# Optimization experiments

Measured on AMD Instinct MI355X. Metric: run time of the kernel, lower is better.

## Reference

```python
import jax, jax.numpy as jnp
import numpy as np

B, S, D, H = 4, 2048, 512, 8
HD = D // H
POOL_HEADS = 8


def setup_inputs() -> dict:
    key = jax.random.key(0)
    ks = iter(jax.random.split(key, 32))
    p = {}
    p['x'] = jax.random.normal(next(ks), (B, S, D), dtype=jnp.float32)
    p['mask'] = jnp.zeros((B, S), dtype=jnp.float32)  # key_padding_mask (1.0 = padded)
    s = 1.0 / np.sqrt(D)
    for layer in ('1', '2'):
        for name in ('q', 'k', 'v', 'o'):
            p[f'{name}{layer}_w'] = jax.random.normal(next(ks), (D, D), dtype=jnp.float32) * s
            p[f'{name}{layer}_b'] = jnp.zeros((D,), dtype=jnp.float32)
    p['ln1_g'] = jnp.ones((D,), jnp.float32); p['ln1_b'] = jnp.zeros((D,), jnp.float32)
    p['ffn_w1'] = jax.random.normal(next(ks), (D, D), dtype=jnp.float32) * s
    p['ffn_b1'] = jnp.zeros((D,), jnp.float32)
    p['ffn_w2'] = jax.random.normal(next(ks), (D, D), dtype=jnp.float32) * s
    p['ffn_b2'] = jnp.zeros((D,), jnp.float32)
    p['ln2_g'] = jnp.ones((D,), jnp.float32); p['ln2_b'] = jnp.zeros((D,), jnp.float32)
    p['pool_w'] = jax.random.normal(next(ks), (D, POOL_HEADS), dtype=jnp.float32) * s
    p['pool_b'] = jnp.zeros((POOL_HEADS,), jnp.float32)
    return p


def _layernorm(x, g, b, eps=1e-5):
    mu = jnp.mean(x, axis=-1, keepdims=True)
    var = jnp.var(x, axis=-1, keepdims=True)
    return (x - mu) * jax.lax.rsqrt(var + eps) * g + b


def _mha(x, mask, qw, qb, kw, kb, vw, vb, ow, ob):
    b, s, d = x.shape
    q = (x @ qw + qb).reshape(b, s, H, HD)
    k = (x @ kw + kb).reshape(b, s, H, HD)
    v = (x @ vw + vb).reshape(b, s, H, HD)
    scores = jnp.einsum('bihd,bjhd->bhij', q, k) / jnp.sqrt(jnp.float32(HD))
    scores = scores - mask[:, None, None, :] * 1e30  # key_padding_mask
    w = jax.nn.softmax(scores, axis=-1)  # dropout is identity at eval
    out = jnp.einsum('bhij,bjhd->bihd', w, v).reshape(b, s, d)
    return out @ ow + ob


def _pool(x, mask, pw, pb):
    alpha = jax.nn.leaky_relu(x @ pw + pb)            # [B,S,POOL_HEADS]
    alpha = alpha + mask[:, :, None] * -1e16
    alpha = jax.nn.softmax(alpha, axis=1)             # softmax over sequence
    # sum over heads of alpha_h * x, then sum over sequence
    return jnp.einsum('bs,bsd->bd', alpha.sum(axis=-1), x)


def reference(x, mask,
              q1_w, q1_b, k1_w, k1_b, v1_w, v1_b, o1_w, o1_b,
              q2_w, q2_b, k2_w, k2_b, v2_w, v2_b, o2_w, o2_b,
              ln1_g, ln1_b, ffn_w1, ffn_b1, ffn_w2, ffn_b2,
              ln2_g, ln2_b, pool_w, pool_b):
    # F.normalize(x, p=2, dim=-1)
    x = x / jnp.maximum(jnp.linalg.norm(x, axis=-1, keepdims=True), 1e-12)
    h = _mha(x, mask, q1_w, q1_b, k1_w, k1_b, v1_w, v1_b, o1_w, o1_b)
    h = _layernorm(h, ln1_g, ln1_b)
    h = jax.nn.relu(h @ ffn_w1 + ffn_b1) @ ffn_w2 + ffn_b2
    h = _mha(h, mask, q2_w, q2_b, k2_w, k2_b, v2_w, v2_b, o2_w, o2_b)
    h = _layernorm(h, ln2_g, ln2_b)
    return _pool(h, mask, pool_w, pool_b)  # [B, D] patch_feature (cls=False -> logit is None)
```

## Files before the change

kernel.cpp:

```cpp
#include <hip/hip_runtime.h>
#include <hip/hip_bf16.h>
#include <stdint.h>

#define DEVI __device__ __forceinline__

typedef float f32x4 __attribute__((ext_vector_type(4)));
typedef short bf16x8 __attribute__((ext_vector_type(8)));

typedef __attribute__((address_space(3))) unsigned int as3_u32;
typedef __attribute__((address_space(1))) unsigned int as1_u32;

DEVI void gload16(const void* g, void* l) {
  __builtin_amdgcn_global_load_lds((const as1_u32*)g, (as3_u32*)l, 16, 0, 0);
}

DEVI unsigned short bf16r(float f) {
  union { float f; unsigned int u; } v; v.f = f;
  unsigned int u = v.u;
  return (unsigned short)((u + 0x7FFFu + ((u >> 16) & 1u)) >> 16);
}

struct PrepArgs {
  const float* w[10];
  const float* b1[3];
  const float* b2[3];
};

__global__ __launch_bounds__(256) void prep_kernel(PrepArgs pa, unsigned short* wt,
                                                   float* qb1, float* qb2) {
  __shared__ float lt[64][65];
  const int slot = blockIdx.z;
  const int n0 = blockIdx.x * 64, k0 = blockIdx.y * 64;
  const float* W = pa.w[slot];
  for (int it = 0; it < 16; it++) {
    int idx = it * 256 + threadIdx.x;
    int kr = idx >> 6, nc = idx & 63;
    lt[kr][nc] = W[(long)(k0 + kr) * 512 + n0 + nc];
  }
  __syncthreads();
  unsigned short* dst = wt + (long)slot * 512 * 512;
  for (int it = 0; it < 16; it++) {
    int idx = it * 256 + threadIdx.x;
    int nr = idx >> 6, kc = idx & 63;
    dst[(long)(n0 + nr) * 512 + k0 + kc] = bf16r(lt[kc][nr]);
  }
  if (blockIdx.x == 0 && blockIdx.y == 0) {
    if (slot < 3) {
      for (int i = threadIdx.x; i < 512; i += 256) qb1[slot * 512 + i] = pa.b1[slot][i];
    } else if (slot >= 6 && slot < 9) {
      for (int i = threadIdx.x; i < 512; i += 256) qb2[(slot - 6) * 512 + i] = pa.b2[slot - 6][i];
    }
  }
}

__global__ __launch_bounds__(256) void l2norm_kernel(const float* __restrict__ x,
                                                     unsigned short* __restrict__ xn) {
  const long row = blockIdx.x;
  const float* xr = x + row * 512;
  float v0 = xr[threadIdx.x], v1 = xr[threadIdx.x + 256];
  float ss = v0 * v0 + v1 * v1;
  #pragma unroll
  for (int off = 32; off > 0; off >>= 1) ss += __shfl_down(ss, off, 64);
  __shared__ float red[4];
  __shared__ float sc[1];
  int w = threadIdx.x >> 6, ln = threadIdx.x & 63;
  if (ln == 0) red[w] = ss;
  __syncthreads();
  if (threadIdx.x == 0) {
    float S = red[0] + red[1] + red[2] + red[3];
    sc[0] = 1.0f / fmaxf(sqrtf(S), 1e-12f);
  }
  __syncthreads();
  float s = sc[0];
  xn[row * 512 + threadIdx.x] = bf16r(v0 * s);
  xn[row * 512 + threadIdx.x + 256] = bf16r(v1 * s);
}

template <int EPI>
__global__ __launch_bounds__(256) void gemm_bt(const unsigned short* __restrict__ A,
                                               const unsigned short* __restrict__ Bt,
                                               const float* __restrict__ bias,
                                               void* __restrict__ Cv, int K, int N) {
  __shared__ unsigned short ldsA[128 * 64];
  __shared__ unsigned short ldsB[128 * 64];
  const int tid = threadIdx.x, w = tid >> 6, ln = tid & 63;
  const int bm = blockIdx.x, bn = blockIdx.y;
  const int wm = (w >> 1) * 64, wn = (w & 1) * 64;
  const f32x4 zf = {0.f, 0.f, 0.f, 0.f};
  f32x4 acc[4][4];
  #pragma unroll
  for (int i = 0; i < 4; i++)
    #pragma unroll
    for (int j = 0; j < 4; j++) acc[i][j] = zf;
  const int r8 = ln >> 3, s8 = ln & 7;
  for (int kt = 0; kt < K; kt += 64) {
    #pragma unroll
    for (int i = 0; i < 4; i++) {
      int row = w * 32 + i * 8 + r8;
      gload16(A + (long)(bm * 128 + row) * K + kt + s8 * 8, &ldsA[(w * 32 + i * 8) * 64]);
      gload16(Bt + (long)(bn * 128 + row) * K + kt + s8 * 8, &ldsB[(w * 32 + i * 8) * 64]);
    }
    __syncthreads();
    #pragma unroll
    for (int kk = 0; kk < 2; kk++) {
      bf16x8 af[4], bfr[4];
      #pragma unroll
      for (int mf = 0; mf < 4; mf++) {
        int row = wm + mf * 16 + (ln & 15);
        af[mf] = *(const bf16x8*)&ldsA[row * 64 + kk * 32 + (ln >> 4) * 8];
      }
      #pragma unroll
      for (int nf = 0; nf < 4; nf++) {
        int row = wn + nf * 16 + (ln & 15);
        bfr[nf] = *(const bf16x8*)&ldsB[row * 64 + kk * 32 + (ln >> 4) * 8];
      }
      #pragma unroll
      for (int mf = 0; mf < 4; mf++)
        #pragma unroll
        for (int nf = 0; nf < 4; nf++)
          acc[mf][nf] = __builtin_amdgcn_mfma_f32_16x16x32_bf16(af[mf], bfr[nf], acc[mf][nf], 0, 0, 0);
    }
    __syncthreads();
  }
  const int g = ln >> 4, c = ln & 15;
  #pragma unroll
  for (int mf = 0; mf < 4; mf++) {
    #pragma unroll
    for (int nf = 0; nf < 4; nf++) {
      int col = bn * 128 + wn + nf * 16 + c;
      float bv = bias[col];
      #pragma unroll
      for (int j = 0; j < 4; j++) {
        long row = bm * 128 + wm + mf * 16 + g * 4 + j;
        float v = acc[mf][nf][j] + bv;
        if (EPI == 2) v = v > 0.f ? v : 0.f;
        if (EPI == 0)
          ((float*)Cv)[row * N + col] = v;
        else
          ((unsigned short*)Cv)[row * N + col] = bf16r(v);
      }
    }
  }
}

__global__ __launch_bounds__(256) void vtrans_kernel(const unsigned short* __restrict__ v,
                                                     unsigned short* __restrict__ vt) {
  __shared__ unsigned short lt[64][72];
  const int bh = blockIdx.x;
  const int st = blockIdx.y * 64;
  const unsigned short* src = v + (long)((bh >> 3) * 2048 + st) * 1536 + (bh & 7) * 64;
  for (int it = 0; it < 16; it++) {
    int idx = it * 256 + threadIdx.x;
    int r = idx >> 6, cc = idx & 63;
    lt[r][cc] = src[(long)r * 1536 + cc];
  }
  __syncthreads();
  unsigned short* dst = vt + (long)bh * 64 * 2048 + st;
  for (int it = 0; it < 16; it++) {
    int idx = it * 256 + threadIdx.x;
    int dr = idx >> 6, sc = idx & 63;
    dst[(long)dr * 2048 + sc] = lt[sc][dr];
  }
}

__global__ __launch_bounds__(256, 4) void attn_split_kernel(
    const unsigned short* __restrict__ qkv,
    const unsigned short* __restrict__ vt,
    const float* __restrict__ mask,
    float* __restrict__ opart,
    float* __restrict__ lpart) {
  const int tid = threadIdx.x, w = tid >> 6, ln = tid & 63;
  const int g = ln >> 4, c = ln & 15;
  const int bh = blockIdx.y, b = bh >> 3, h = bh & 7;
  const int sp = blockIdx.z;
  const int q0 = blockIdx.x * 128 + w * 32;
  const unsigned short* qp = qkv + (long)(b * 2048) * 1536 + h * 64;
  const unsigned short* kp = qp + 512;
  const unsigned short* vtp = vt + (long)bh * 64 * 2048;
  const float* mp = mask + b * 2048;

  __shared__ unsigned short kbuf[2][32 * 64];
  __shared__ unsigned short vbuf[2][64 * 32];
  __shared__ unsigned short pbuf[4 * 16 * 64];
  unsigned short* pb = &pbuf[w * 1024];

  const int jj0 = w * 2;
  auto stage = [&](int buf, int kt) {
    #pragma unroll
    for (int u = 0; u < 2; u++) {
      int jj = jj0 + u;
      if (jj < 4) {
        int r = jj * 8 + (ln >> 3);
        int s = ln & 7;
        gload16(kp + (long)(kt + r) * 1536 + ((s ^ (r & 7)) * 8),
                &kbuf[buf][jj * 512]);
      } else {
        int j = jj - 4;
        int r = j * 16 + (ln >> 2);
        int s = ln & 3;
        gload16(vtp + (long)r * 2048 + kt + ((s ^ ((r >> 1) & 3)) * 8),
                &vbuf[buf][j * 512]);
      }
    }
  };

  const f32x4 zf = {0.f, 0.f, 0.f, 0.f};
  bf16x8 qf[2][2];
  #pragma unroll
  for (int qi = 0; qi < 2; qi++)
    #pragma unroll
    for (int kk = 0; kk < 2; kk++)
      qf[qi][kk] = *(const bf16x8*)(qp + (long)(q0 + qi * 16 + c) * 1536 + kk * 32 + g * 8);

  f32x4 of[4][2];
  #pragma unroll
  for (int i = 0; i < 4; i++)
    #pragma unroll
    for (int j = 0; j < 2; j++) of[i][j] = zf;
  float lsum[2] = {0.f, 0.f};

  const int kt0 = sp * 1024;
  stage(0, kt0);
  __syncthreads();

  for (int it = 0; it < 32; it++) {
    const int kt = kt0 + it * 32;
    const int cur = it & 1;
    if (it + 1 < 32) stage(cur ^ 1, kt + 32);
    float mval = mp[kt + (ln & 31)];
    bf16x8 kf[2][2];
    #pragma unroll
    for (int ki = 0; ki < 2; ki++)
      #pragma unroll
      for (int kk = 0; kk < 2; kk++)
        kf[ki][kk] = *(const bf16x8*)&kbuf[cur][(ki * 16 + c) * 64 + (((kk * 4 + g) ^ (c & 7)) * 8)];
    bf16x8 vf[4];
    #pragma unroll
    for (int hf = 0; hf < 4; hf++)
      vf[hf] = *(const bf16x8*)&vbuf[cur][(hf * 16 + c) * 32 + ((g ^ ((c >> 1) & 3)) * 8)];
    f32x4 st[2][2];
    #pragma unroll
    for (int ki = 0; ki < 2; ki++)
      #pragma unroll
      for (int qi = 0; qi < 2; qi++) {
        f32x4 t0 = __builtin_amdgcn_mfma_f32_16x16x32_bf16(kf[ki][0], qf[qi][0], zf, 0, 0, 0);
        st[ki][qi] = __builtin_amdgcn_mfma_f32_16x16x32_bf16(kf[ki][1], qf[qi][1], t0, 0, 0, 0);
      }
    float madj[2][4];
    #pragma unroll
    for (int ki = 0; ki < 2; ki++)
      #pragma unroll
      for (int j = 0; j < 4; j++) madj[ki][j] = 0.f;
    if (__any(mval != 0.f)) {
      #pragma unroll
      for (int ki = 0; ki < 2; ki++)
        #pragma unroll
        for (int j = 0; j < 4; j++)
          madj[ki][j] = -1.4426950408889634e30f * __shfl(mval, ki * 16 + g * 4 + j, 64);
    }
    const float SC = 0.18033688011112042f;
    #pragma unroll
    for (int qi = 0; qi < 2; qi++) {
      #pragma unroll
      for (int ki = 0; ki < 2; ki++) {
        float e0 = __builtin_amdgcn_exp2f(st[ki][qi][0] * SC + madj[ki][0]);
        float e1 = __builtin_amdgcn_exp2f(st[ki][qi][1] * SC + madj[ki][1]);
        float e2 = __builtin_amdgcn_exp2f(st[ki][qi][2] * SC + madj[ki][2]);
        float e3 = __builtin_amdgcn_exp2f(st[ki][qi][3] * SC + madj[ki][3]);
        lsum[qi] += (e0 + e1) + (e2 + e3);
        __hip_bfloat162 h01 = __float22bfloat162_rn(make_float2(e0, e1));
        __hip_bfloat162 h23 = __float22bfloat162_rn(make_float2(e2, e3));
        uint2 pk;
        pk.x = *(unsigned int*)&h01;
        pk.y = *(unsigned int*)&h23;
        int slot = (qi * 4 + ki * 2 + (g >> 1)) ^ (c & 7);
        *(uint2*)&pb[c * 64 + slot * 8 + (g & 1) * 4] = pk;
      }
    }
    bf16x8 pfr[2];
    #pragma unroll
    for (int qi = 0; qi < 2; qi++) {
      int slot = (qi * 4 + g) ^ (c & 7);
      pfr[qi] = *(const bf16x8*)&pb[c * 64 + slot * 8];
    }
    #pragma unroll
    for (int hf = 0; hf < 4; hf++)
      #pragma unroll
      for (int qi = 0; qi < 2; qi++)
        of[hf][qi] = __builtin_amdgcn_mfma_f32_16x16x32_bf16(vf[hf], pfr[qi], of[hf][qi], 0, 0, 0);
    __syncthreads();
  }
  #pragma unroll
  for (int qi = 0; qi < 2; qi++) {
    lsum[qi] += __shfl_xor(lsum[qi], 16, 64);
    lsum[qi] += __shfl_xor(lsum[qi], 32, 64);
  }
  float* ob = opart + (long)(sp * 32 + bh) * 2048 * 64;
  #pragma unroll
  for (int qi = 0; qi < 2; qi++) {
    long row = q0 + qi * 16 + c;
    #pragma unroll
    for (int hf = 0; hf < 4; hf++)
      *(f32x4*)(ob + row * 64 + hf * 16 + g * 4) = of[hf][qi];
  }
  if (g == 0) {
    #pragma unroll
    for (int qi = 0; qi < 2; qi++)
      lpart[(long)(sp * 32 + bh) * 2048 + q0 + qi * 16 + c] = lsum[qi];
  }
}

__global__ __launch_bounds__(256) void attn_combine(const float* __restrict__ opart,
                                                    const float* __restrict__ lpart,
                                                    unsigned short* __restrict__ ao) {
  const long row = blockIdx.x;
  const int b = (int)(row >> 11), q = (int)(row & 2047);
  #pragma unroll
  for (int half = 0; half < 2; half++) {
    int col = threadIdx.x + half * 256;
    int h = col >> 6, hd = col & 63;
    int bh = b * 8 + h;
    float l = lpart[(long)bh * 2048 + q] + lpart[(long)(32 + bh) * 2048 + q];
    long i0 = ((long)bh * 2048 + q) * 64 + hd;
    long i1 = ((long)(32 + bh) * 2048 + q) * 64 + hd;
    float v = (opart[i0] + opart[i1]) / l;
    ao[row * 512 + col] = bf16r(v);
  }
}

template <int OUTF>
__global__ __launch_bounds__(256) void ln_kernel(const float* __restrict__ in,
                                                 const float* __restrict__ gam,
                                                 const float* __restrict__ bet,
                                                 void* __restrict__ out) {
  const long row = blockIdx.x;
  const float* x = in + row * 512;
  float v0 = x[threadIdx.x], v1 = x[threadIdx.x + 256];
  float s = v0 + v1, ss = v0 * v0 + v1 * v1;
  #pragma unroll
  for (int off = 32; off > 0; off >>= 1) {
    s += __shfl_down(s, off, 64);
    ss += __shfl_down(ss, off, 64);
  }
  __shared__ float red[8];
  __shared__ float mv[2];
  int w = threadIdx.x >> 6, ln = threadIdx.x & 63;
  if (ln == 0) { red[w] = s; red[w + 4] = ss; }
  __syncthreads();
  if (threadIdx.x == 0) {
    float S = red[0] + red[1] + red[2] + red[3];
    float SS = red[4] + red[5] + red[6] + red[7];
    float mu = S * (1.f / 512.f);
    float var = SS * (1.f / 512.f) - mu * mu;
    mv[0] = mu;
    mv[1] = rsqrtf(var + 1e-5f);
  }
  __syncthreads();
  float mu = mv[0], rs = mv[1];
  float o0 = (v0 - mu) * rs * gam[threadIdx.x] + bet[threadIdx.x];
  float o1 = (v1 - mu) * rs * gam[threadIdx.x + 256] + bet[threadIdx.x + 256];
  if (OUTF == 0) {
    ((unsigned short*)out)[row * 512 + threadIdx.x] = bf16r(o0);
    ((unsigned short*)out)[row * 512 + threadIdx.x + 256] = bf16r(o1);
  } else {
    ((float*)out)[row * 512 + threadIdx.x] = o0;
    ((float*)out)[row * 512 + threadIdx.x + 256] = o1;
  }
}

__global__ __launch_bounds__(256) void alpha_kernel(const float* __restrict__ h,
                                                    const float* __restrict__ pw,
                                                    const float* __restrict__ pbias,
                                                    const float* __restrict__ mask,
                                                    float* __restrict__ alpha) {
  int w = threadIdx.x >> 6, ln = threadIdx.x & 63;
  long row = (long)blockIdx.x * 4 + w;
  float p[8];
  #pragma unroll
  for (int k = 0; k < 8; k++) p[k] = 0.f;
  #pragma unroll
  for (int it = 0; it < 8; it++) {
    int d = it * 64 + ln;
    float xv = h[row * 512 + d];
    const float* wr = pw + d * 8;
    #pragma unroll
    for (int k = 0; k < 8; k++) p[k] += xv * wr[k];
  }
  #pragma unroll
  for (int off = 32; off > 0; off >>= 1)
    #pragma unroll
    for (int k = 0; k < 8; k++) p[k] += __shfl_down(p[k], off, 64);
  if (ln == 0) {
    float mterm = mask[row] * (-1e16f);
    #pragma unroll
    for (int k = 0; k < 8; k++) {
      float a = p[k] + pbias[k];
      a = a < 0.f ? 0.01f * a : a;
      alpha[row * 8 + k] = a + mterm;
    }
  }
}

__global__ __launch_bounds__(256) void stats_kernel(const float* __restrict__ alpha,
                                                    float* __restrict__ stats) {
  int b = blockIdx.x >> 3, ph = blockIdx.x & 7;
  const float* a = alpha + (long)b * 2048 * 8 + ph;
  __shared__ float rr[4];
  __shared__ float mm[1];
  int w = threadIdx.x >> 6, ln = threadIdx.x & 63;
  float m = -1e38f;
  for (int s = threadIdx.x; s < 2048; s += 256) m = fmaxf(m, a[(long)s * 8]);
  #pragma unroll
  for (int off = 32; off > 0; off >>= 1) m = fmaxf(m, __shfl_down(m, off, 64));
  if (ln == 0) rr[w] = m;
  __syncthreads();
  if (threadIdx.x == 0) mm[0] = fmaxf(fmaxf(rr[0], rr[1]), fmaxf(rr[2], rr[3]));
  __syncthreads();
  float M = mm[0];
  float sum = 0.f;
  for (int s = threadIdx.x; s < 2048; s += 256) sum += __expf(a[(long)s * 8] - M);
  #pragma unroll
  for (int off = 32; off > 0; off >>= 1) sum += __shfl_down(sum, off, 64);
  __syncthreads();
  if (ln == 0) rr[w] = sum;
  __syncthreads();
  if (threadIdx.x == 0) {
    stats[blockIdx.x * 2] = M;
    stats[blockIdx.x * 2 + 1] = rr[0] + rr[1] + rr[2] + rr[3];
  }
}

__global__ __launch_bounds__(256) void pool_kernel(const float* __restrict__ h,
                                                   const float* __restrict__ alpha,
                                                   const float* __restrict__ stats,
                                                   float* __restrict__ partial) {
  int b = blockIdx.x >> 3, sc = blockIdx.x & 7;
  int s0 = sc * 256;
  __shared__ float wb[256];
  {
    long s = s0 + threadIdx.x;
    const float* a = alpha + ((long)b * 2048 + s) * 8;
    float wsum = 0.f;
    #pragma unroll
    for (int ph = 0; ph < 8; ph++) {
      float M = stats[(b * 8 + ph) * 2], Sm = stats[(b * 8 + ph) * 2 + 1];
      wsum += __expf(a[ph] - M) / Sm;
    }
    wb[threadIdx.x] = wsum;
  }
  __syncthreads();
  float a0 = 0.f, a1 = 0.f;
  const float* hb = h + ((long)b * 2048 + s0) * 512;
  for (int i = 0; i < 256; i++) {
    float wv = wb[i];
    a0 += wv * hb[(long)i * 512 + threadIdx.x];
    a1 += wv * hb[(long)i * 512 + threadIdx.x + 256];
  }
  partial[(long)blockIdx.x * 512 + threadIdx.x] = a0;
  partial[(long)blockIdx.x * 512 + threadIdx.x + 256] = a1;
}

__global__ __launch_bounds__(256) void pool_final(const float* __restrict__ partial,
                                                  float* __restrict__ out) {
  int b = blockIdx.x;
  float a0 = 0.f, a1 = 0.f;
  #pragma unroll
  for (int sc = 0; sc < 8; sc++) {
    a0 += partial[(long)(b * 8 + sc) * 512 + threadIdx.x];
    a1 += partial[(long)(b * 8 + sc) * 512 + threadIdx.x + 256];
  }
  out[b * 512 + threadIdx.x] = a0;
  out[b * 512 + threadIdx.x + 256] = a1;
}

extern "C" void kernel_launch(void* const* d_in, const int* in_sizes, int n_in,
                              void* d_out, int out_size, void* d_ws, size_t ws_size,
                              hipStream_t stream) {
  (void)in_sizes; (void)n_in; (void)out_size;
  if (ws_size < 92274688UL) return;

  const float* x    = (const float*)d_in[0];
  const float* mask = (const float*)d_in[1];
  const float* q1w = (const float*)d_in[2];  const float* q1b = (const float*)d_in[3];
  const float* k1w = (const float*)d_in[4];  const float* k1b = (const float*)d_in[5];
  const float* v1w = (const float*)d_in[6];  const float* v1b = (const float*)d_in[7];
  const float* o1w = (const float*)d_in[8];  const float* o1b = (const float*)d_in[9];
  const float* q2w = (const float*)d_in[10]; const float* q2b = (const float*)d_in[11];
  const float* k2w = (const float*)d_in[12]; const float* k2b = (const float*)d_in[13];
  const float* v2w = (const float*)d_in[14]; const float* v2b = (const float*)d_in[15];
  const float* o2w = (const float*)d_in[16]; const float* o2b = (const float*)d_in[17];
  const float* ln1g = (const float*)d_in[18]; const float* ln1b = (const float*)d_in[19];
  const float* fw1 = (const float*)d_in[20]; const float* fb1 = (const float*)d_in[21];
  const float* fw2 = (const float*)d_in[22]; const float* fb2 = (const float*)d_in[23];
  const float* ln2g = (const float*)d_in[24]; const float* ln2b = (const float*)d_in[25];
  const float* poolw = (const float*)d_in[26]; const float* poolb = (const float*)d_in[27];

  char* ws = (char*)d_ws;
  unsigned short* Wt  = (unsigned short*)(ws + 0);
  float* qb1          = (float*)(ws + 5242880);
  float* qb2          = (float*)(ws + 5249024);
  float* stats        = (float*)(ws + 5255168);
  float* alpha        = (float*)(ws + 5255424);
  float* partial      = (float*)(ws + 5517568);
  unsigned short* qkv = (unsigned short*)(ws + 8388608);
  unsigned short* vt  = (unsigned short*)(ws + 33554432);
  unsigned short* ao  = (unsigned short*)(ws + 41943040);
  float* t            = (float*)(ws + 50331648);
  unsigned short* xn  = (unsigned short*)(ws + 67108864);
  unsigned short* h1  = (unsigned short*)(ws + 75497472);
  unsigned short* f   = (unsigned short*)(ws + 83886080);
  unsigned short* h2  = xn;
  float* opart        = (float*)(ws + 50331648);
  float* lpart        = (float*)(ws + 83886080);

  PrepArgs pa;
  pa.w[0] = q1w; pa.w[1] = k1w; pa.w[2] = v1w; pa.w[3] = o1w; pa.w[4] = fw1;
  pa.w[5] = fw2; pa.w[6] = q2w; pa.w[7] = k2w; pa.w[8] = v2w; pa.w[9] = o2w;
  pa.b1[0] = q1b; pa.b1[1] = k1b; pa.b1[2] = v1b;
  pa.b2[0] = q2b; pa.b2[1] = k2b; pa.b2[2] = v2b;

  prep_kernel<<<dim3(8, 8, 10), 256, 0, stream>>>(pa, Wt, qb1, qb2);
  l2norm_kernel<<<8192, 256, 0, stream>>>(x, xn);

  gemm_bt<1><<<dim3(64, 12), 256, 0, stream>>>(xn, Wt, qb1, qkv, 512, 1536);
  vtrans_kernel<<<dim3(32, 32), 256, 0, stream>>>(qkv + 1024, vt);
  attn_split_kernel<<<dim3(16, 32, 2), 256, 0, stream>>>(qkv, vt, mask, opart, lpart);
  attn_combine<<<8192, 256, 0, stream>>>(opart, lpart, ao);
  gemm_bt<0><<<dim3(64, 4), 256, 0, stream>>>(ao, Wt + 3L * 512 * 512, o1b, t, 512, 512);
  ln_kernel<0><<<8192, 256, 0, stream>>>(t, ln1g, ln1b, h1);
  gemm_bt<2><<<dim3(64, 4), 256, 0, stream>>>(h1, Wt + 4L * 512 * 512, fb1, f, 512, 512);
  gemm_bt<1><<<dim3(64, 4), 256, 0, stream>>>(f, Wt + 5L * 512 * 512, fb2, h2, 512, 512);

  gemm_bt<1><<<dim3(64, 12), 256, 0, stream>>>(h2, Wt + 6L * 512 * 512, qb2, qkv, 512, 1536);
  vtrans_kernel<<<dim3(32, 32), 256, 0, stream>>>(qkv + 1024, vt);
  attn_split_kernel<<<dim3(16, 32, 2), 256, 0, stream>>>(qkv, vt, mask, opart, lpart);
  attn_combine<<<8192, 256, 0, stream>>>(opart, lpart, ao);
  gemm_bt<0><<<dim3(64, 4), 256, 0, stream>>>(ao, Wt + 9L * 512 * 512, o2b, t, 512, 512);
  ln_kernel<1><<<8192, 256, 0, stream>>>(t, ln2g, ln2b, t);

  alpha_kernel<<<2048, 256, 0, stream>>>(t, poolw, poolb, mask, alpha);
  stats_kernel<<<32, 256, 0, stream>>>(alpha, stats);
  pool_kernel<<<32, 256, 0, stream>>>(t, alpha, stats, partial);
  pool_final<<<4, 256, 0, stream>>>(partial, (float*)d_out);
}
```

Measured before the change: 309.6 us.

## Fuse V transpose into QKV GEMM, widen attention K tile, add 64-wide GEMM

The QKV GEMM now writes V columns directly in transposed [b,h,hd,s] layout through a new epilogue mode, which removes the separate vtrans kernel and its extra read and write of V. The attention kernel stages 64 keys per buffer instead of 32. That halves the number of barriers and stage calls, but doubles the LDS used for K and V. The 512-wide GEMMs switch to a 128x64 tile variant, which doubles the grid from 256 to 512 blocks for better CU occupancy at the cost of less data reuse per block.

```diff
diff --git a/kernel.cpp b/kernel.cpp
--- a/kernel.cpp
+++ b/kernel.cpp
@@ -80,7 +80,8 @@
 __global__ __launch_bounds__(256) void gemm_bt(const unsigned short* __restrict__ A,
                                                const unsigned short* __restrict__ Bt,
                                                const float* __restrict__ bias,
-                                               void* __restrict__ Cv, int K, int N) {
+                                               void* __restrict__ Cv, int K, int N,
+                                               unsigned short* __restrict__ vtout) {
   __shared__ unsigned short ldsA[128 * 64];
   __shared__ unsigned short ldsB[128 * 64];
   const int tid = threadIdx.x, w = tid >> 6, ln = tid & 63;
@@ -128,6 +129,85 @@
     #pragma unroll
     for (int nf = 0; nf < 4; nf++) {
       int col = bn * 128 + wn + nf * 16 + c;
+      float bv = bias[col];
+      if (EPI == 3 && col >= 1024) {
+        long row0 = bm * 128 + wm + mf * 16 + g * 4;
+        int b = (int)(row0 >> 11), s = (int)(row0 & 2047);
+        int vc = col - 1024, h = vc >> 6, hd = vc & 63;
+        ushort4 o;
+        o.x = bf16r(acc[mf][nf][0] + bv);
+        o.y = bf16r(acc[mf][nf][1] + bv);
+        o.z = bf16r(acc[mf][nf][2] + bv);
+        o.w = bf16r(acc[mf][nf][3] + bv);
+        *(ushort4*)(vtout + ((long)((b * 8 + h) * 64 + hd)) * 2048 + s) = o;
+      } else {
+        #pragma unroll
+        for (int j = 0; j < 4; j++) {
+          long row = bm * 128 + wm + mf * 16 + g * 4 + j;
+          float v = acc[mf][nf][j] + bv;
+          if (EPI == 2) v = v > 0.f ? v : 0.f;
+          if (EPI == 0)
+            ((float*)Cv)[row * N + col] = v;
+          else
+            ((unsigned short*)Cv)[row * N + col] = bf16r(v);
+        }
+      }
+    }
+  }
+}
+
+template <int EPI>
+__global__ __launch_bounds__(256) void gemm_bt64(const unsigned short* __restrict__ A,
+                                                 const unsigned short* __restrict__ Bt,
+                                                 const float* __restrict__ bias,
+                                                 void* __restrict__ Cv, int K, int N) {
+  __shared__ unsigned short ldsA[128 * 64];
+  __shared__ unsigned short ldsB[64 * 64];
+  const int tid = threadIdx.x, w = tid >> 6, ln = tid & 63;
+  const int bm = blockIdx.x, bn = blockIdx.y;
+  const int wm = (w >> 1) * 64, wn = (w & 1) * 32;
+  const f32x4 zf = {0.f, 0.f, 0.f, 0.f};
+  f32x4 acc[4][2];
+  #pragma unroll
+  for (int i = 0; i < 4; i++)
+    #pragma unroll
+    for (int j = 0; j < 2; j++) acc[i][j] = zf;
+  const int r8 = ln >> 3, s8 = ln & 7;
+  for (int kt = 0; kt < K; kt += 64) {
+    #pragma unroll
+    for (int i = 0; i < 6; i++) {
+      int jj = w * 6 + i;
+      if (jj < 16) {
+        gload16(A + (long)(bm * 128 + jj * 8 + r8) * K + kt + s8 * 8, &ldsA[jj * 512]);
+      } else {
+        int jb = jj - 16;
+        gload16(Bt + (long)(bn * 64 + jb * 8 + r8) * K + kt + s8 * 8, &ldsB[jb * 512]);
+      }
+    }
+    __syncthreads();
+    #pragma unroll
+    for (int kk = 0; kk < 2; kk++) {
+      bf16x8 af[4], bfr[2];
+      #pragma unroll
+      for (int mf = 0; mf < 4; mf++)
+        af[mf] = *(const bf16x8*)&ldsA[(wm + mf * 16 + (ln & 15)) * 64 + kk * 32 + (ln >> 4) * 8];
+      #pragma unroll
+      for (int nf = 0; nf < 2; nf++)
+        bfr[nf] = *(const bf16x8*)&ldsB[(wn + nf * 16 + (ln & 15)) * 64 + kk * 32 + (ln >> 4) * 8];
+      #pragma unroll
+      for (int mf = 0; mf < 4; mf++)
+        #pragma unroll
+        for (int nf = 0; nf < 2; nf++)
+          acc[mf][nf] = __builtin_amdgcn_mfma_f32_16x16x32_bf16(af[mf], bfr[nf], acc[mf][nf], 0, 0, 0);
+    }
+    __syncthreads();
+  }
+  const int g = ln >> 4, c = ln & 15;
+  #pragma unroll
+  for (int mf = 0; mf < 4; mf++) {
+    #pragma unroll
+    for (int nf = 0; nf < 2; nf++) {
+      int col = bn * 64 + wn + nf * 16 + c;
       float bv = bias[col];
       #pragma unroll
       for (int j = 0; j < 4; j++) {
@@ -140,26 +220,6 @@
           ((unsigned short*)Cv)[row * N + col] = bf16r(v);
       }
     }
-  }
-}
-
-__global__ __launch_bounds__(256) void vtrans_kernel(const unsigned short* __restrict__ v,
-                                                     unsigned short* __restrict__ vt) {
-  __shared__ unsigned short lt[64][72];
-  const int bh = blockIdx.x;
-  const int st = blockIdx.y * 64;
-  const unsigned short* src = v + (long)((bh >> 3) * 2048 + st) * 1536 + (bh & 7) * 64;
-  for (int it = 0; it < 16; it++) {
-    int idx = it * 256 + threadIdx.x;
-    int r = idx >> 6, cc = idx & 63;
-    lt[r][cc] = src[(long)r * 1536 + cc];
-  }
-  __syncthreads();
-  unsigned short* dst = vt + (long)bh * 64 * 2048 + st;
-  for (int it = 0; it < 16; it++) {
-    int idx = it * 256 + threadIdx.x;
-    int dr = idx >> 6, sc = idx & 63;
-    dst[(long)dr * 2048 + sc] = lt[sc][dr];
   }
 }
 
@@ -179,27 +239,24 @@
   const unsigned short* vtp = vt + (long)bh * 64 * 2048;
   const float* mp = mask + b * 2048;
 
-  __shared__ unsigned short kbuf[2][32 * 64];
-  __shared__ unsigned short vbuf[2][64 * 32];
+  __shared__ unsigned short kbuf[2][64 * 64];
+  __shared__ unsigned short vbuf[2][64 * 64];
   __shared__ unsigned short pbuf[4 * 16 * 64];
   unsigned short* pb = &pbuf[w * 1024];
 
-  const int jj0 = w * 2;
+  const int r8 = ln >> 3, s8 = ln & 7;
   auto stage = [&](int buf, int kt) {
     #pragma unroll
-    for (int u = 0; u < 2; u++) {
-      int jj = jj0 + u;
-      if (jj < 4) {
-        int r = jj * 8 + (ln >> 3);
-        int s = ln & 7;
-        gload16(kp + (long)(kt + r) * 1536 + ((s ^ (r & 7)) * 8),
+    for (int u = 0; u < 4; u++) {
+      int jj = w * 4 + u;
+      if (jj < 8) {
+        int r = jj * 8 + r8;
+        gload16(kp + (long)(kt + r) * 1536 + ((s8 ^ (r & 7)) * 8),
                 &kbuf[buf][jj * 512]);
       } else {
-        int j = jj - 4;
-        int r = j * 16 + (ln >> 2);
-        int s = ln & 3;
-        gload16(vtp + (long)r * 2048 + kt + ((s ^ ((r >> 1) & 3)) * 8),
-                &vbuf[buf][j * 512]);
+        int r = (jj - 8) * 8 + r8;
+        gload16(vtp + (long)r * 2048 + kt + ((s8 ^ (r & 7)) * 8),
+                &vbuf[buf][(jj - 8) * 512]);
       }
     }
   };
@@ -223,71 +280,75 @@
   stage(0, kt0);
   __syncthreads();
 
-  for (int it = 0; it < 32; it++) {
-    const int kt = kt0 + it * 32;
+  for (int it = 0; it < 16; it++) {
+    const int kt = kt0 + it * 64;
     const int cur = it & 1;
-    if (it + 1 < 32) stage(cur ^ 1, kt + 32);
-    float mval = mp[kt + (ln & 31)];
-    bf16x8 kf[2][2];
-    #pragma unroll
-    for (int ki = 0; ki < 2; ki++)
-      #pragma unroll
-      for (int kk = 0; kk < 2; kk++)
-        kf[ki][kk] = *(const bf16x8*)&kbuf[cur][(ki * 16 + c) * 64 + (((kk * 4 + g) ^ (c & 7)) * 8)];
-    bf16x8 vf[4];
-    #pragma unroll
-    for (int hf = 0; hf < 4; hf++)
-      vf[hf] = *(const bf16x8*)&vbuf[cur][(hf * 16 + c) * 32 + ((g ^ ((c >> 1) & 3)) * 8)];
-    f32x4 st[2][2];
-    #pragma unroll
-    for (int ki = 0; ki < 2; ki++)
+    if (it + 1 < 16) stage(cur ^ 1, kt + 64);
+    #pragma unroll
+    for (int s = 0; s < 2; s++) {
+      const int ks = kt + s * 32;
+      float mval = mp[ks + (ln & 31)];
+      bf16x8 kf[2][2];
+      #pragma unroll
+      for (int ki = 0; ki < 2; ki++)
+        #pragma unroll
+        for (int kk = 0; kk < 2; kk++)
+          kf[ki][kk] = *(const bf16x8*)&kbuf[cur][(s * 32 + ki * 16 + c) * 64 + (((kk * 4 + g) ^ (c & 7)) * 8)];
+      bf16x8 vf[4];
+      #pragma unroll
+      for (int hf = 0; hf < 4; hf++)
+        vf[hf] = *(const bf16x8*)&vbuf[cur][(hf * 16 + c) * 64 + (((s * 4 + g) ^ (c & 7)) * 8)];
+      f32x4 st[2][2];
+      #pragma unroll
+      for (int ki = 0; ki < 2; ki++)
+        #pragma unroll
+        for (int qi = 0; qi < 2; qi++) {
+          f32x4 t0 = __builtin_amdgcn_mfma_f32_16x16x32_bf16(kf[ki][0], qf[qi][0], zf, 0, 0, 0);
+          st[ki][qi] = __builtin_amdgcn_mfma_f32_16x16x32_bf16(kf[ki][1], qf[qi][1], t0, 0, 0, 0);
+        }
+      float madj[2][4];
+      #pragma unroll
+      for (int ki = 0; ki < 2; ki++)
+        #pragma unroll
+        for (int j = 0; j < 4; j++) madj[ki][j] = 0.f;
+      if (__any(mval != 0.f)) {
+        #pragma unroll
+        for (int ki = 0; ki < 2; ki++)
+          #pragma unroll
+          for (int j = 0; j < 4; j++)
+            madj[ki][j] = -1.4426950408889634e30f * __shfl(mval, ki * 16 + g * 4 + j, 64);
+      }
+      const float SC = 0.18033688011112042f;
       #pragma unroll
       for (int qi = 0; qi < 2; qi++) {
-        f32x4 t0 = __builtin_amdgcn_mfma_f32_16x16x32_bf16(kf[ki][0], qf[qi][0], zf, 0, 0, 0);
-        st[ki][qi] = __builtin_amdgcn_mfma_f32_16x16x32_bf16(kf[ki][1], qf[qi][1], t0, 0, 0, 0);
-      }
-    float madj[2][4];
-    #pragma unroll
-    for (int ki = 0; ki < 2; ki++)
-      #pragma unroll
-      for (int j = 0; j < 4; j++) madj[ki][j] = 0.f;
-    if (__any(mval != 0.f)) {
-      #pragma unroll
-      for (int ki = 0; ki < 2; ki++)
-        #pragma unroll
-        for (int j = 0; j < 4; j++)
-          madj[ki][j] = -1.4426950408889634e30f * __shfl(mval, ki * 16 + g * 4 + j, 64);
-    }
-    const float SC = 0.18033688011112042f;
-    #pragma unroll
-    for (int qi = 0; qi < 2; qi++) {
-      #pragma unroll
-      for (int ki = 0; ki < 2; ki++) {
-        float e0 = __builtin_amdgcn_exp2f(st[ki][qi][0] * SC + madj[ki][0]);
-        float e1 = __builtin_amdgcn_exp2f(st[ki][qi][1] * SC + madj[ki][1]);
-        float e2 = __builtin_amdgcn_exp2f(st[ki][qi][2] * SC + madj[ki][2]);
-        float e3 = __builtin_amdgcn_exp2f(st[ki][qi][3] * SC + madj[ki][3]);
-        lsum[qi] += (e0 + e1) + (e2 + e3);
-        __hip_bfloat162 h01 = __float22bfloat162_rn(make_float2(e0, e1));
-        __hip_bfloat162 h23 = __float22bfloat162_rn(make_float2(e2, e3));
-        uint2 pk;
-        pk.x = *(unsigned int*)&h01;
-        pk.y = *(unsigned int*)&h23;
-        int slot = (qi * 4 + ki * 2 + (g >> 1)) ^ (c & 7);
-        *(uint2*)&pb[c * 64 + slot * 8 + (g & 1) * 4] = pk;
-      }
-    }
-    bf16x8 pfr[2];
-    #pragma unroll
-    for (int qi = 0; qi < 2; qi++) {
-      int slot = (qi * 4 + g) ^ (c & 7);
-      pfr[qi] = *(const bf16x8*)&pb[c * 64 + slot * 8];
-    }
-    #pragma unroll
-    for (int hf = 0; hf < 4; hf++)
-      #pragma unroll
-      for (int qi = 0; qi < 2; qi++)
-        of[hf][qi] = __builtin_amdgcn_mfma_f32_16x16x32_bf16(vf[hf], pfr[qi], of[hf][qi], 0, 0, 0);
+        #pragma unroll
+        for (int ki = 0; ki < 2; ki++) {
+          float e0 = __builtin_amdgcn_exp2f(st[ki][qi][0] * SC + madj[ki][0]);
+          float e1 = __builtin_amdgcn_exp2f(st[ki][qi][1] * SC + madj[ki][1]);
+          float e2 = __builtin_amdgcn_exp2f(st[ki][qi][2] * SC + madj[ki][2]);
+          float e3 = __builtin_amdgcn_exp2f(st[ki][qi][3] * SC + madj[ki][3]);
+          lsum[qi] += (e0 + e1) + (e2 + e3);
+          __hip_bfloat162 h01 = __float22bfloat162_rn(make_float2(e0, e1));
+          __hip_bfloat162 h23 = __float22bfloat162_rn(make_float2(e2, e3));
+          uint2 pk;
+          pk.x = *(unsigned int*)&h01;
+          pk.y = *(unsigned int*)&h23;
+          int slot = (qi * 4 + ki * 2 + (g >> 1)) ^ (c & 7);
+          *(uint2*)&pb[c * 64 + slot * 8 + (g & 1) * 4] = pk;
+        }
+      }
+      bf16x8 pfr[2];
+      #pragma unroll
+      for (int qi = 0; qi < 2; qi++) {
+        int slot = (qi * 4 + g) ^ (c & 7);
+        pfr[qi] = *(const bf16x8*)&pb[c * 64 + slot * 8];
+      }
+      #pragma unroll
+      for (int hf = 0; hf < 4; hf++)
+        #pragma unroll
+        for (int qi = 0; qi < 2; qi++)
+          of[hf][qi] = __builtin_amdgcn_mfma_f32_16x16x32_bf16(vf[hf], pfr[qi], of[hf][qi], 0, 0, 0);
+    }
     __syncthreads();
   }
   #pragma unroll
@@ -522,20 +583,18 @@
   prep_kernel<<<dim3(8, 8, 10), 256, 0, stream>>>(pa, Wt, qb1, qb2);
   l2norm_kernel<<<8192, 256, 0, stream>>>(x, xn);
 
-  gemm_bt<1><<<dim3(64, 12), 256, 0, stream>>>(xn, Wt, qb1, qkv, 512, 1536);
-  vtrans_kernel<<<dim3(32, 32), 256, 0, stream>>>(qkv + 1024, vt);
+  gemm_bt<3><<<dim3(64, 12), 256, 0, stream>>>(xn, Wt, qb1, qkv, 512, 1536, vt);
   attn_split_kernel<<<dim3(16, 32, 2), 256, 0, stream>>>(qkv, vt, mask, opart, lpart);
   attn_combine<<<8192, 256, 0, stream>>>(opart, lpart, ao);
-  gemm_bt<0><<<dim3(64, 4), 256, 0, stream>>>(ao, Wt + 3L * 512 * 512, o1b, t, 512, 512);
+  gemm_bt64<0><<<dim3(64, 8), 256, 0, stream>>>(ao, Wt + 3L * 512 * 512, o1b, t, 512, 512);
   ln_kernel<0><<<8192, 256, 0, stream>>>(t, ln1g, ln1b, h1);
-  gemm_bt<2><<<dim3(64, 4), 256, 0, stream>>>(h1, Wt + 4L * 512 * 512, fb1, f, 512, 512);
-  gemm_bt<1><<<dim3(64, 4), 256, 0, stream>>>(f, Wt + 5L * 512 * 512, fb2, h2, 512, 512);
-
-  gemm_bt<1><<<dim3(64, 12), 256, 0, stream>>>(h2, Wt + 6L * 512 * 512, qb2, qkv, 512, 1536);
-  vtrans_kernel<<<dim3(32, 32), 256, 0, stream>>>(qkv + 1024, vt);
+  gemm_bt64<2><<<dim3(64, 8), 256, 0, stream>>>(h1, Wt + 4L * 512 * 512, fb1, f, 512, 512);
+  gemm_bt64<1><<<dim3(64, 8), 256, 0, stream>>>(f, Wt + 5L * 512 * 512, fb2, h2, 512, 512);
+
+  gemm_bt<3><<<dim3(64, 12), 256, 0, stream>>>(h2, Wt + 6L * 512 * 512, qb2, qkv, 512, 1536, vt);
   attn_split_kernel<<<dim3(16, 32, 2), 256, 0, stream>>>(qkv, vt, mask, opart, lpart);
   attn_combine<<<8192, 256, 0, stream>>>(opart, lpart, ao);
-  gemm_bt<0><<<dim3(64, 4), 256, 0, stream>>>(ao, Wt + 9L * 512 * 512, o2b, t, 512, 512);
+  gemm_bt64<0><<<dim3(64, 8), 256, 0, stream>>>(ao, Wt + 9L * 512 * 512, o2b, t, 512, 512);
   ln_kernel<1><<<8192, 256, 0, stream>>>(t, ln2g, ln2b, t);
 
   alpha_kernel<<<2048, 256, 0, stream>>>(t, poolw, poolb, mask, alpha);
```

Measured after the change: 376.5 us. +21.6%, slower.
